# Kernel tuning notes

Measured on AMD Instinct MI355X. Metric: run time of the kernel, lower is better.

## Reference

```python
import jax, jax.numpy as jnp
import numpy as np

B, H, W, C = 8, 64, 64, 256
CF = C // 8  # f/g projection channels


def setup_inputs() -> dict:
    key = jax.random.key(0)
    ks = jax.random.split(key, 7)
    glorot = lambda k, shape, fan_in, fan_out: jax.random.uniform(
        k, shape, jnp.float32, -1.0, 1.0) * np.sqrt(6.0 / (fan_in + fan_out))
    return {
        "x": jax.random.normal(ks[0], (B, H, W, C), jnp.float32),
        "kernel_f": glorot(ks[1], (1, 1, C, CF), C, CF),
        "kernel_g": glorot(ks[2], (1, 1, C, CF), C, CF),
        "kernel_h": glorot(ks[3], (1, 1, C, C), C, C),
        "bias_f": jnp.zeros((CF,), jnp.float32),
        "bias_g": jnp.zeros((CF,), jnp.float32),
        "bias_h": jnp.zeros((C,), jnp.float32),
        "gamma": jnp.zeros((1,), jnp.float32),
    }


def reference(x, kernel_f, kernel_g, kernel_h, bias_f, bias_g, bias_h, gamma):
    b, h, w, c = x.shape
    n = h * w
    xf = x.reshape(b, n, c)  # hw_flatten; 1x1 conv == per-pixel GEMM
    f = jnp.einsum('bnc,cd->bnd', xf, kernel_f[0, 0]) + bias_f  # [B,N,C/8]
    g = jnp.einsum('bnc,cd->bnd', xf, kernel_g[0, 0]) + bias_g  # [B,N,C/8]
    hh = jnp.einsum('bnc,cd->bnd', xf, kernel_h[0, 0]) + bias_h  # [B,N,C]
    s = jnp.einsum('bid,bjd->bij', g, f)  # matmul(g, f^T): [B,N,N]
    beta = jax.nn.softmax(s, axis=-1)
    o = jnp.einsum('bij,bjc->bic', beta, hh)  # [B,N,C]
    return gamma * o.reshape(b, h, w, c) + x
```

## Files before the change

kernel.cpp:

```cpp
#include <hip/hip_runtime.h>
#include <hip/hip_bf16.h>

#define BATCH 8
#define NTOK 4096
#define CH 256
#define CF 32
#define KVBLK 128
#define NITER (NTOK / KVBLK)

typedef float v4f __attribute__((ext_vector_type(4)));
typedef float v16f __attribute__((ext_vector_type(16)));
typedef short v8s __attribute__((ext_vector_type(8)));

static __device__ __forceinline__ ushort f2bf(float f) {
    union { float f; uint u; } v; v.f = f;
    uint u = v.u;
    uint r = (u + 0x7fffu + ((u >> 16) & 1u)) >> 16;
    return (ushort)r;
}

static __device__ __forceinline__ uint cvt_pk(float lo, float hi) {
    uint r;
    asm("v_cvt_pk_bf16_f32 %0, %1, %2" : "=v"(r) : "v"(lo), "v"(hi));
    return r;
}

static __device__ __forceinline__ void plswap(uint& a, uint& b) {
    asm("v_permlane32_swap_b32 %0, %1" : "+v"(a), "+v"(b));
}

static __device__ __forceinline__ void gload16(const void* g, void* l) {
    __builtin_amdgcn_global_load_lds(
        (const __attribute__((address_space(1))) unsigned int*)g,
        (__attribute__((address_space(3))) unsigned int*)l, 16, 0, 0);
}

#define MFMA16(a, b, c) __builtin_amdgcn_mfma_f32_16x16x32_bf16(a, b, c, 0, 0, 0)
#define MFMA32(a, b, c) __builtin_amdgcn_mfma_f32_32x32x16_bf16(a, b, c, 0, 0, 0)

__global__ __launch_bounds__(256) void prep_weights(
    const float* __restrict__ kf, const float* __restrict__ kg,
    const float* __restrict__ kh,
    ushort* __restrict__ wfT, ushort* __restrict__ wgT, ushort* __restrict__ whT) {
    __shared__ float tile[64][33];
    int bid = blockIdx.x;
    const float* src; ushort* dst; int cols, k0, c0;
    if (bid < 32)      { src = kh; dst = whT; cols = 256; k0 = (bid >> 3) * 64; c0 = (bid & 7) * 32; }
    else if (bid < 36) { src = kf; dst = wfT; cols = 32;  k0 = (bid - 32) * 64; c0 = 0; }
    else               { src = kg; dst = wgT; cols = 32;  k0 = (bid - 36) * 64; c0 = 0; }
    int t = threadIdx.x;
    int kr = t >> 2, cb = (t & 3) * 8;
#pragma unroll
    for (int j = 0; j < 8; ++j) tile[kr][cb + j] = src[(size_t)(k0 + kr) * cols + c0 + cb + j];
    __syncthreads();
    int c = t >> 3, kc = (t & 7) * 8;
    ushort tmp[8];
#pragma unroll
    for (int j = 0; j < 8; ++j) tmp[j] = f2bf(tile[kc + j][c]);
    *(uint4*)(dst + (size_t)(c0 + c) * CH + k0 + kc) = *(uint4*)tmp;
}

__global__ __launch_bounds__(256) void proj_fgx(
    const float* __restrict__ x, const ushort* __restrict__ wfT,
    const ushort* __restrict__ wgT, const float* __restrict__ bf,
    const float* __restrict__ bg,
    ushort* __restrict__ fo, ushort* __restrict__ go, ushort* __restrict__ XT) {
    __shared__ __align__(16) ushort xl[64 * 256];
    __shared__ __align__(16) ushort wl[2][32 * 256];
    int tid = threadIdx.x;
    int lane = tid & 63, w = tid >> 6;
    int row15 = lane & 15, g4 = lane >> 4;
    int n0 = blockIdx.x * 64;
    int batch = n0 >> 12, nn0 = n0 & (NTOK - 1);

#pragma unroll
    for (int i = 0; i < 8; ++i) {
        int id = i * 256 + tid;
        int sel = id >> 10, r = (id >> 5) & 31, s = id & 31;
        const ushort* src = (sel ? wgT : wfT) + r * CH + ((s ^ (r & 7)) << 3);
        gload16(src, (char*)&wl[0][0] + id * 16);
    }
#pragma unroll
    for (int i = 0; i < 8; ++i) {
        int id = i * 256 + tid;
        int n = id >> 5, cc = id & 31;
        const float* xp = x + (size_t)(n0 + n) * CH + cc * 8;
        float4 a0 = ((const float4*)xp)[0], a1 = ((const float4*)xp)[1];
        uint4 pv;
        pv.x = cvt_pk(a0.x, a0.y); pv.y = cvt_pk(a0.z, a0.w);
        pv.z = cvt_pk(a1.x, a1.y); pv.w = cvt_pk(a1.z, a1.w);
        *(uint4*)((char*)xl + n * 512 + ((cc ^ (n & 7)) << 4)) = pv;
    }
    asm volatile("s_waitcnt vmcnt(0)" ::: "memory");
    __syncthreads();

    v4f accF[2] = {}, accG[2] = {};
    int nrow = w * 16 + row15;
    for (int ks = 0; ks < 8; ++ks) {
        v8s xf = *(const v8s*)((char*)xl + nrow * 512 + (((ks * 4 + g4) ^ (nrow & 7)) << 4));
#pragma unroll
        for (int ct = 0; ct < 2; ++ct) {
            int wr = ct * 16 + row15;
            int wb = wr * 512 + (((ks * 4 + g4) ^ (wr & 7)) << 4);
            v8s bwf = *(const v8s*)((char*)&wl[0][0] + wb);
            v8s bwg = *(const v8s*)((char*)&wl[1][0] + wb);
            accF[ct] = MFMA16(xf, bwf, accF[ct]);
            accG[ct] = MFMA16(xf, bwg, accG[ct]);
        }
    }
#pragma unroll
    for (int ct = 0; ct < 2; ++ct)
#pragma unroll
        for (int r = 0; r < 4; ++r) {
            int n = n0 + w * 16 + g4 * 4 + r;
            int cf = ct * 16 + row15;
            fo[(size_t)n * CF + cf] = f2bf(accF[ct][r] + bf[cf]);
            go[(size_t)n * CF + cf] = f2bf(accG[ct][r] + bg[cf]);
        }

    ushort* XTb = XT + (size_t)batch * CH * NTOK;
    int c = tid;
#pragma unroll
    for (int i = 0; i < 8; ++i) {
        ushort tmp[8];
#pragma unroll
        for (int j = 0; j < 8; ++j) {
            int row = i * 8 + j;
            int chunk = (c >> 3) ^ j;
            tmp[j] = xl[row * 256 + chunk * 8 + (c & 7)];
        }
        *(uint4*)(XTb + (size_t)c * NTOK + nn0 + i * 8) = *(uint4*)tmp;
    }
}

__global__ __launch_bounds__(512, 1) void flash_attn(
    const ushort* __restrict__ fbuf, const ushort* __restrict__ gbuf,
    const ushort* __restrict__ XT,
    ushort* __restrict__ PX, float* __restrict__ lsw) {
    __shared__ __align__(16) ushort lds_v[2][32768];
    __shared__ float lsx[4][32];

    int tid = threadIdx.x;
    int lane = tid & 63, w = tid >> 6;
    int row31 = lane & 31, h = lane >> 5;
    int batch = blockIdx.x & 7;
    int qg = w >> 1, kh = w & 1;
    int q0 = (blockIdx.x >> 3) * 128 + qg * 32;

    const ushort* fB = fbuf + (size_t)batch * NTOK * CF;
    const ushort* gB = gbuf + (size_t)batch * NTOK * CF;
    const ushort* vB = XT + (size_t)batch * CH * NTOK;

    int crow = tid >> 4;
    int koffe = ((tid & 15) ^ (crow & 15)) << 3;
    const ushort* vpb = vB + (size_t)crow * NTOK + koffe;

#define STAGE(buf) do {                                                    \
        _Pragma("unroll")                                                  \
        for (int i_ = 0; i_ < 8; ++i_)                                     \
            gload16(vpb + (size_t)(i_ * 32) * NTOK,                        \
                    (char*)&lds_v[buf][0] + (i_ * 512 + tid) * 16);        \
    } while (0)

    const ushort* kp = fB + (size_t)(kh * 64 + row31) * CF + h * 8;

    int voff[2][2];
#pragma unroll
    for (int kt = 0; kt < 2; ++kt)
#pragma unroll
        for (int j = 0; j < 2; ++j) {
            int ch = kh * 8 + (kt * 2 + j) * 2 + h;
            voff[kt][j] = row31 * 256 + ((ch ^ (row31 & 15)) << 4);
        }

    v8s bq[2];
    bq[0] = *(const v8s*)(gB + (size_t)(q0 + row31) * CF + h * 8);
    bq[1] = *(const v8s*)(gB + (size_t)(q0 + row31) * CF + 16 + h * 8);

    float lsum = 0.f;
    v16f acc[8] = {};
    const v16f z16 = {};

    v8s k00 = *(const v8s*)kp;
    v8s k01 = *(const v8s*)(kp + 16);
    v8s k10 = *(const v8s*)(kp + 32 * CF);
    v8s k11 = *(const v8s*)(kp + 32 * CF + 16);
    kp += KVBLK * CF;
    STAGE(0); vpb += KVBLK;

    for (int t = 0; t < NITER; ++t) {
        int cur = t & 1;
        __builtin_amdgcn_s_barrier();
        v8s n00 = {}, n01 = {}, n10 = {}, n11 = {};
        if (t + 1 < NITER) {
            STAGE(cur ^ 1); vpb += KVBLK;
            n00 = *(const v8s*)kp;
            n01 = *(const v8s*)(kp + 16);
            n10 = *(const v8s*)(kp + 32 * CF);
            n11 = *(const v8s*)(kp + 32 * CF + 16);
            kp += KVBLK * CF;
            asm volatile("s_waitcnt vmcnt(12)" ::: "memory");
        } else {
            asm volatile("s_waitcnt vmcnt(0)" ::: "memory");
        }
        __builtin_amdgcn_s_barrier();

        const char* vb = (const char*)&lds_v[cur][0];

        v16f s0, s1;
        s0 = MFMA32(k00, bq[0], z16); s0 = MFMA32(k01, bq[1], s0);
        s1 = MFMA32(k10, bq[0], z16); s1 = MFMA32(k11, bq[1], s1);

        float psum = 0.f;
#pragma unroll
        for (int r = 0; r < 16; ++r) {
            s0[r] = __builtin_amdgcn_exp2f(s0[r] * 1.44269504f - 34.6246924f);
            s1[r] = __builtin_amdgcn_exp2f(s1[r] * 1.44269504f - 34.6246924f);
            psum += s0[r] + s1[r];
        }
        psum += __shfl_xor(psum, 32);
        lsum += psum;

        __builtin_amdgcn_s_setprio(1);
#pragma unroll
        for (int kt = 0; kt < 2; ++kt)
#pragma unroll
            for (int j = 0; j < 2; ++j) {
                int R = j * 8;
                uint a0, a1, b0, b1;
                if (kt == 0) {
                    a0 = cvt_pk(s0[R + 0], s0[R + 1]); a1 = cvt_pk(s0[R + 2], s0[R + 3]);
                    b0 = cvt_pk(s0[R + 4], s0[R + 5]); b1 = cvt_pk(s0[R + 6], s0[R + 7]);
                } else {
                    a0 = cvt_pk(s1[R + 0], s1[R + 1]); a1 = cvt_pk(s1[R + 2], s1[R + 3]);
                    b0 = cvt_pk(s1[R + 4], s1[R + 5]); b1 = cvt_pk(s1[R + 6], s1[R + 7]);
                }
                plswap(a0, b0);
                plswap(a1, b1);
                union { v8s v; uint u[4]; } pu;
                pu.u[0] = a0; pu.u[1] = a1; pu.u[2] = b0; pu.u[3] = b1;
#pragma unroll
                for (int ct = 0; ct < 8; ++ct) {
                    v8s bv = *(const v8s*)(vb + voff[kt][j] + ct * 8192);
                    acc[ct] = MFMA32(pu.v, bv, acc[ct]);
                }
            }
        __builtin_amdgcn_s_setprio(0);
        k00 = n00; k01 = n01; k10 = n10; k11 = n11;
    }
#undef STAGE

    float* mbuf = (float*)&lds_v[0][0];
    int p = qg;
    if (kh == 1) {
        lsx[p][row31] = lsum;
#pragma unroll
        for (int ct = 0; ct < 4; ++ct)
#pragma unroll
            for (int r = 0; r < 16; ++r) {
                int qrow = (r & 3) + 8 * (r >> 2) + 4 * h;
                mbuf[p * 4096 + qrow * 128 + ct * 32 + row31] = acc[ct][r];
            }
    }
    __syncthreads();
    if (kh == 0) {
        float ltot = lsum + lsx[p][row31];
        if (h == 0) lsw[batch * NTOK + q0 + row31] = ltot;
#pragma unroll
        for (int ct = 0; ct < 4; ++ct)
#pragma unroll
            for (int r = 0; r < 16; ++r) {
                int qrow = (r & 3) + 8 * (r >> 2) + 4 * h;
                float val = acc[ct][r] + mbuf[p * 4096 + qrow * 128 + ct * 32 + row31];
                PX[((size_t)batch * NTOK + q0 + qrow) * CH + ct * 32 + row31] = f2bf(val);
            }
    }
    __syncthreads();
    if (kh == 1) {
#pragma unroll
        for (int ct = 4; ct < 8; ++ct)
#pragma unroll
            for (int r = 0; r < 16; ++r) {
                int qrow = (r & 3) + 8 * (r >> 2) + 4 * h;
                mbuf[p * 4096 + qrow * 128 + (ct - 4) * 32 + row31] = acc[ct][r];
            }
    }
    __syncthreads();
    if (kh == 0) {
#pragma unroll
        for (int ct = 4; ct < 8; ++ct)
#pragma unroll
            for (int r = 0; r < 16; ++r) {
                int qrow = (r & 3) + 8 * (r >> 2) + 4 * h;
                float val = acc[ct][r] + mbuf[p * 4096 + qrow * 128 + (ct - 4) * 32 + row31];
                PX[((size_t)batch * NTOK + q0 + qrow) * CH + ct * 32 + row31] = f2bf(val);
            }
    }
}

__global__ __launch_bounds__(256) void gemm_h(
    const ushort* __restrict__ PX, const ushort* __restrict__ whT,
    const float* __restrict__ lsw, const float* __restrict__ bh,
    const float* __restrict__ x, const float* __restrict__ gamma,
    float* __restrict__ out) {
    __shared__ __align__(16) ushort pxl[64 * 256];
    __shared__ __align__(16) ushort wll[64 * 256];
    int tid = threadIdx.x;
    int lane = tid & 63, w = tid >> 6;
    int row15 = lane & 15, g4 = lane >> 4;
    int n0 = blockIdx.x * 64, c0 = blockIdx.y * 64;

#pragma unroll
    for (int i = 0; i < 8; ++i) {
        int id = i * 256 + tid;
        int n = id >> 5, s = id & 31;
        gload16(PX + (size_t)(n0 + n) * CH + ((s ^ (n & 7)) << 3),
                (char*)pxl + id * 16);
    }
#pragma unroll
    for (int i = 0; i < 8; ++i) {
        int id = i * 256 + tid;
        int c = id >> 5, s = id & 31;
        gload16(whT + (size_t)(c0 + c) * CH + ((s ^ (c & 7)) << 3),
                (char*)wll + id * 16);
    }
    asm volatile("s_waitcnt vmcnt(0)" ::: "memory");
    __syncthreads();

    v4f acc[4] = {};
    int wr = w * 16 + row15;
    for (int ks = 0; ks < 8; ++ks) {
        v8s bw = *(const v8s*)((char*)wll + wr * 512 + (((ks * 4 + g4) ^ (wr & 7)) << 4));
#pragma unroll
        for (int nt = 0; nt < 4; ++nt) {
            int nr = nt * 16 + row15;
            v8s af = *(const v8s*)((char*)pxl + nr * 512 + (((ks * 4 + g4) ^ (nr & 7)) << 4));
            acc[nt] = MFMA16(af, bw, acc[nt]);
        }
    }

    float gm = gamma[0];
    int c = c0 + w * 16 + row15;
    float bhc = gm * bh[c];
#pragma unroll
    for (int nt = 0; nt < 4; ++nt)
#pragma unroll
        for (int r = 0; r < 4; ++r) {
            int n = n0 + nt * 16 + g4 * 4 + r;
            float li = 1.0f / lsw[n];
            size_t idx = (size_t)n * CH + c;
            out[idx] = gm * acc[nt][r] * li + bhc + x[idx];
        }
}

extern "C" void kernel_launch(void* const* d_in, const int* in_sizes, int n_in,
                              void* d_out, int out_size, void* d_ws, size_t ws_size,
                              hipStream_t stream) {
    const float* x  = (const float*)d_in[0];
    const float* kf = (const float*)d_in[1];
    const float* kg = (const float*)d_in[2];
    const float* kh = (const float*)d_in[3];
    const float* bf = (const float*)d_in[4];
    const float* bg = (const float*)d_in[5];
    const float* bh = (const float*)d_in[6];
    const float* gm = (const float*)d_in[7];
    float* out = (float*)d_out;

    char* ws = (char*)d_ws;
    ushort* wfT = (ushort*)(ws);
    ushort* wgT = (ushort*)(ws + 16384);
    ushort* whT = (ushort*)(ws + 32768);
    ushort* fo  = (ushort*)(ws + 163840);
    ushort* go  = (ushort*)(ws + 163840 + 2097152);
    ushort* XT  = (ushort*)(ws + 4358144);
    ushort* PX  = (ushort*)(ws + 4358144 + 16777216);
    float*  lsw = (float* )(ws + 4358144 + 33554432);

    hipLaunchKernelGGL(prep_weights, dim3(40), dim3(256), 0, stream, kf, kg, kh, wfT, wgT, whT);
    hipLaunchKernelGGL(proj_fgx, dim3(512), dim3(256), 0, stream,
                       x, wfT, wgT, bf, bg, fo, go, XT);
    hipLaunchKernelGGL(flash_attn, dim3(256), dim3(512), 0, stream, fo, go, XT, PX, lsw);
    hipLaunchKernelGGL(gemm_h, dim3(512, 4), dim3(256), 0, stream,
                       PX, whT, lsw, bh, x, gm, out);
}
```

Before: 127.3 us.

## Software-pipeline QK score and exp computation one iteration ahead of PV MFMAs

Computes the next block's QK^T scores and exp2 at the end of the current iteration, so they overlap the V staging loads and come right after the PV MFMAs instead of sitting on the critical path after the barrier. K loads are issued before the V stage, with adjusted vmcnt waits and sched_barriers to pin the instruction order. This holds extra live registers for s0/s1 across iterations, which can raise register pressure and lower occupancy. It also depends on the vmcnt counts staying correct.

```diff
diff --git a/kernel.cpp b/kernel.cpp
--- a/kernel.cpp
+++ b/kernel.cpp
@@ -186,19 +186,37 @@
     v8s k10 = *(const v8s*)(kp + 32 * CF);
     v8s k11 = *(const v8s*)(kp + 32 * CF + 16);
     kp += KVBLK * CF;
+    __builtin_amdgcn_sched_barrier(0);
     STAGE(0); vpb += KVBLK;
+    __builtin_amdgcn_sched_barrier(0);
+    asm volatile("s_waitcnt vmcnt(8)" ::: "memory");
+    __builtin_amdgcn_sched_barrier(0);
+
+    v16f s0, s1;
+    s0 = MFMA32(k00, bq[0], z16); s0 = MFMA32(k01, bq[1], s0);
+    s1 = MFMA32(k10, bq[0], z16); s1 = MFMA32(k11, bq[1], s1);
+    float psumc = 0.f;
+#pragma unroll
+    for (int r = 0; r < 16; ++r) {
+        s0[r] = __builtin_amdgcn_exp2f(s0[r] * 1.44269504f - 34.6246924f);
+        s1[r] = __builtin_amdgcn_exp2f(s1[r] * 1.44269504f - 34.6246924f);
+        psumc += s0[r] + s1[r];
+    }
+    psumc += __shfl_xor(psumc, 32);
 
     for (int t = 0; t < NITER; ++t) {
         int cur = t & 1;
         __builtin_amdgcn_s_barrier();
-        v8s n00 = {}, n01 = {}, n10 = {}, n11 = {};
+        v8s n00, n01, n10, n11;
         if (t + 1 < NITER) {
-            STAGE(cur ^ 1); vpb += KVBLK;
             n00 = *(const v8s*)kp;
             n01 = *(const v8s*)(kp + 16);
             n10 = *(const v8s*)(kp + 32 * CF);
             n11 = *(const v8s*)(kp + 32 * CF + 16);
             kp += KVBLK * CF;
+            __builtin_amdgcn_sched_barrier(0);
+            STAGE(cur ^ 1); vpb += KVBLK;
+            __builtin_amdgcn_sched_barrier(0);
             asm volatile("s_waitcnt vmcnt(12)" ::: "memory");
         } else {
             asm volatile("s_waitcnt vmcnt(0)" ::: "memory");
@@ -206,20 +224,6 @@
         __builtin_amdgcn_s_barrier();
 
         const char* vb = (const char*)&lds_v[cur][0];
-
-        v16f s0, s1;
-        s0 = MFMA32(k00, bq[0], z16); s0 = MFMA32(k01, bq[1], s0);
-        s1 = MFMA32(k10, bq[0], z16); s1 = MFMA32(k11, bq[1], s1);
-
-        float psum = 0.f;
-#pragma unroll
-        for (int r = 0; r < 16; ++r) {
-            s0[r] = __builtin_amdgcn_exp2f(s0[r] * 1.44269504f - 34.6246924f);
-            s1[r] = __builtin_amdgcn_exp2f(s1[r] * 1.44269504f - 34.6246924f);
-            psum += s0[r] + s1[r];
-        }
-        psum += __shfl_xor(psum, 32);
-        lsum += psum;
 
         __builtin_amdgcn_s_setprio(1);
 #pragma unroll
@@ -246,7 +250,23 @@
                 }
             }
         __builtin_amdgcn_s_setprio(0);
-        k00 = n00; k01 = n01; k10 = n10; k11 = n11;
+        lsum += psumc;
+
+        if (t + 1 < NITER) {
+            asm volatile("s_waitcnt vmcnt(8)" ::: "memory");
+            __builtin_amdgcn_sched_barrier(0);
+            s0 = MFMA32(n00, bq[0], z16); s0 = MFMA32(n01, bq[1], s0);
+            s1 = MFMA32(n10, bq[0], z16); s1 = MFMA32(n11, bq[1], s1);
+            float ps = 0.f;
+#pragma unroll
+            for (int r = 0; r < 16; ++r) {
+                s0[r] = __builtin_amdgcn_exp2f(s0[r] * 1.44269504f - 34.6246924f);
+                s1[r] = __builtin_amdgcn_exp2f(s1[r] * 1.44269504f - 34.6246924f);
+                ps += s0[r] + s1[r];
+            }
+            ps += __shfl_xor(ps, 32);
+            psumc = ps;
+        }
     }
 #undef STAGE
 
```

Measured after the change: 129.2 us. No clear change (+1.5%).
